# Optimization experiments

Measured on AMD Instinct MI355X. Metric: run time of the kernel, lower is better.

## Reference

```python
import jax, jax.numpy as jnp
import numpy as np


def setup_inputs() -> dict:
    key = jax.random.key(0)
    x = jax.random.normal(key, (2_000_000, 9), dtype=jnp.float32)
    return {"x": x}


def reference(x):
    # Symmetric orthogonalization onto SO(3):
    #   M = U S V^T ;  R = U diag(1, 1, det(U V^T)) V^T
    m = x.reshape(-1, 3, 3)                      # [N, 3, 3]
    u, s, vh = jnp.linalg.svd(m, full_matrices=False)  # u:[N,3,3], vh:[N,3,3] (= V^T)
    det = jnp.linalg.det(jnp.matmul(u, vh))      # [N]
    # Flip last column of U by sign of det to land in SO(3) (det = +1)
    u_fixed = jnp.concatenate(
        [u[:, :, :2], u[:, :, 2:] * det[:, None, None]], axis=2
    )
    return jnp.matmul(u_fixed, vh)               # [N, 3, 3]
```

## Files before the change

kernel.cpp:

```cpp
#include <hip/hip_runtime.h>

#define TPB 256
#define MPW 128
#define FPW (MPW * 9)
#define F4PW (FPW / 4)
#define MPB (MPW * 4)

typedef float v2f __attribute__((ext_vector_type(2)));
typedef int   v2i __attribute__((ext_vector_type(2)));

static __device__ __forceinline__ v2f sqrt2(v2f a){
    v2f r; r.x = __builtin_amdgcn_sqrtf(a.x); r.y = __builtin_amdgcn_sqrtf(a.y); return r;
}
static __device__ __forceinline__ v2f rsq2(v2f a){
    v2f r; r.x = __builtin_amdgcn_rsqf(a.x); r.y = __builtin_amdgcn_rsqf(a.y); return r;
}
static __device__ __forceinline__ v2f csign2(v2f x, v2f y){
    v2f r; r.x = copysignf(x.x, y.x); r.y = copysignf(x.y, y.y); return r;
}
static __device__ __forceinline__ v2f fabs2(v2f x){
    v2f r; r.x = fabsf(x.x); r.y = fabsf(x.y); return r;
}
static __device__ __forceinline__ v2f sel2(v2i m, v2f a, v2f b){
    v2f r; r.x = m.x ? a.x : b.x; r.y = m.y ? a.y : b.y; return r;
}
static __device__ __forceinline__ void rot2(v2f &p, v2f &q, v2f c, v2f s){
    v2f x = p, y = q; p = c*x - s*y; q = s*x + c*y;
}

static __device__ __forceinline__ void jrot2(v2f &app, v2f &aqq, v2f &apq,
                                             v2f &arp, v2f &arq,
                                             v2f &v0p, v2f &v1p, v2f &v2p,
                                             v2f &v0q, v2f &v1q, v2f &v2q)
{
    v2f d   = aqq - app;
    v2f w   = apq + apq;
    v2f nrm = d*d + w*w;
    v2f rr  = sqrt2(nrm);
    v2f sr  = csign2(rr, d);
    v2f den = d + sr;
    v2f inv = rsq2(den*den + w*w);
    v2f c   = fabs2(den) * inv;
    v2f s   = w * csign2(inv, den);
    v2i tiny = nrm < (v2f)1e-30f;
    c = sel2(tiny, (v2f)1.0f, c);
    s = sel2(tiny, (v2f)0.0f, s);
    v2f sum = app + aqq;
    v2f lo  = 0.5f*(sum - sr);
    app = lo; aqq = sum - lo; apq = (v2f)0.0f;
    rot2(arp, arq, c, s);
    rot2(v0p, v0q, c, s);
    rot2(v1p, v1q, c, s);
    rot2(v2p, v2q, c, s);
}

static __device__ __forceinline__ void solve2(
    v2f m00, v2f m01, v2f m02,
    v2f m10, v2f m11, v2f m12,
    v2f m20, v2f m21, v2f m22,
    v2f &r00, v2f &r01, v2f &r02,
    v2f &r10, v2f &r11, v2f &r12,
    v2f &r20, v2f &r21, v2f &r22)
{
    v2f a00 = m00*m00 + m10*m10 + m20*m20;
    v2f a11 = m01*m01 + m11*m11 + m21*m21;
    v2f a22 = m02*m02 + m12*m12 + m22*m22;
    v2f a01 = m00*m01 + m10*m11 + m20*m21;
    v2f a02 = m00*m02 + m10*m12 + m20*m22;
    v2f a12 = m01*m02 + m11*m12 + m21*m22;

    v2f v00 = (v2f)1.0f, v01 = (v2f)0.0f, v02 = (v2f)0.0f;
    v2f v10 = (v2f)0.0f, v11 = (v2f)1.0f, v12 = (v2f)0.0f;
    v2f v20 = (v2f)0.0f, v21 = (v2f)0.0f, v22 = (v2f)1.0f;

    #pragma unroll
    for (int sw = 0; sw < 3; ++sw) {
        jrot2(a00, a11, a01, a02, a12, v00, v10, v20, v01, v11, v21);
        jrot2(a00, a22, a02, a01, a12, v00, v10, v20, v02, v12, v22);
        jrot2(a11, a22, a12, a01, a02, v01, v11, v21, v02, v12, v22);
    }

    v2f t;
    {
        v2i c01 = a00 < a11;
        t = a00; a00 = sel2(c01, a11, a00); a11 = sel2(c01, t, a11);
        t = v00; v00 = sel2(c01, v01, v00); v01 = sel2(c01, -t, v01);
        t = v10; v10 = sel2(c01, v11, v10); v11 = sel2(c01, -t, v11);
        t = v20; v20 = sel2(c01, v21, v20); v21 = sel2(c01, -t, v21);
    }
    {
        v2i c02 = a00 < a22;
        t = a00; a00 = sel2(c02, a22, a00); a22 = sel2(c02, t, a22);
        t = v00; v00 = sel2(c02, v02, v00); v02 = sel2(c02, -t, v02);
        t = v10; v10 = sel2(c02, v12, v10); v12 = sel2(c02, -t, v12);
        t = v20; v20 = sel2(c02, v22, v20); v22 = sel2(c02, -t, v22);
    }
    {
        v2i c12 = a11 < a22;
        t = a11; a11 = sel2(c12, a22, a11); a22 = sel2(c12, t, a22);
        t = v01; v01 = sel2(c12, v02, v01); v02 = sel2(c12, -t, v02);
        t = v11; v11 = sel2(c12, v12, v11); v12 = sel2(c12, -t, v12);
        t = v21; v21 = sel2(c12, v22, v21); v22 = sel2(c12, -t, v22);
    }

    v2f b00 = m00*v00 + m01*v10 + m02*v20;
    v2f b10 = m10*v00 + m11*v10 + m12*v20;
    v2f b20 = m20*v00 + m21*v10 + m22*v20;
    v2f b01 = m00*v01 + m01*v11 + m02*v21;
    v2f b11 = m10*v01 + m11*v11 + m12*v21;
    v2f b21 = m20*v01 + m21*v11 + m22*v21;

    v2f n1 = b00*b00 + b10*b10 + b20*b20;
    v2f i1 = rsq2(n1);
    v2i ok1 = n1 > (v2f)1e-30f;
    i1 = sel2(ok1, i1, (v2f)0.0f);
    v2f u00 = b00*i1, u10 = b10*i1, u20 = b20*i1;

    v2f d12 = b01*u00 + b11*u10 + b21*u20;
    v2f q0 = b01 - d12*u00;
    v2f q1 = b11 - d12*u10;
    v2f q2 = b21 - d12*u20;
    v2f n2 = q0*q0 + q1*q1 + q2*q2;
    v2f i2 = rsq2(n2);
    v2i ok2 = n2 > (v2f)1e-30f;
    i2 = sel2(ok2, i2, (v2f)0.0f);
    v2f u01 = q0*i2, u11 = q1*i2, u21 = q2*i2;

    v2f u02 = u10*u21 - u20*u11;
    v2f u12 = u20*u01 - u00*u21;
    v2f u22 = u00*u11 - u10*u01;

    r00 = u00*v00 + u01*v01 + u02*v02;
    r01 = u00*v10 + u01*v11 + u02*v12;
    r02 = u00*v20 + u01*v21 + u02*v22;
    r10 = u10*v00 + u11*v01 + u12*v02;
    r11 = u10*v10 + u11*v11 + u12*v12;
    r12 = u10*v20 + u11*v21 + u12*v22;
    r20 = u20*v00 + u21*v01 + u22*v02;
    r21 = u20*v10 + u21*v11 + u22*v12;
    r22 = u20*v20 + u21*v21 + u22*v22;
}

static __device__ __forceinline__ float4 ld_f4(const float* __restrict__ x, long f, long ntotf){
    if (f + 4 <= ntotf) return *(const float4*)(x + f);
    float4 r = make_float4(0.f, 0.f, 0.f, 0.f);
    if (f     < ntotf) r.x = x[f];
    if (f + 1 < ntotf) r.y = x[f + 1];
    if (f + 2 < ntotf) r.z = x[f + 2];
    if (f + 3 < ntotf) r.w = x[f + 3];
    return r;
}
static __device__ __forceinline__ void st_f4(float* __restrict__ o, long f, float4 v, long ntotf){
    if (f + 4 <= ntotf) { *(float4*)(o + f) = v; return; }
    if (f     < ntotf) o[f]     = v.x;
    if (f + 1 < ntotf) o[f + 1] = v.y;
    if (f + 2 < ntotf) o[f + 2] = v.z;
    if (f + 3 < ntotf) o[f + 3] = v.w;
}

__global__ __launch_bounds__(TPB) void svdo_kernel(const float* __restrict__ x,
                                                   float* __restrict__ out,
                                                   int nmat)
{
    __shared__ float lds[4][FPW];
    const int lane = threadIdx.x & 63;
    const int wv   = threadIdx.x >> 6;
    const long mbase = (long)blockIdx.x * MPB + (long)wv * MPW;
    const long fb    = mbase * 9;
    const long ntotf = (long)nmat * 9;
    float* L = lds[wv];

    #pragma unroll
    for (int k = 0; k < 5; ++k) {
        const int idx = lane + k * 64;
        if (idx < F4PW) {
            float4 v = ld_f4(x, fb + (long)idx * 4, ntotf);
            *(float4*)&L[idx * 4] = v;
        }
    }
    asm volatile("s_waitcnt lgkmcnt(0)" ::: "memory");
    __builtin_amdgcn_sched_barrier(0);

    const float* p0 = &L[lane * 9];
    const float* p1 = &L[(lane + 64) * 9];
    v2f m00 = {p0[0], p1[0]}, m01 = {p0[1], p1[1]}, m02 = {p0[2], p1[2]};
    v2f m10 = {p0[3], p1[3]}, m11 = {p0[4], p1[4]}, m12 = {p0[5], p1[5]};
    v2f m20 = {p0[6], p1[6]}, m21 = {p0[7], p1[7]}, m22 = {p0[8], p1[8]};

    v2f r00, r01, r02, r10, r11, r12, r20, r21, r22;
    solve2(m00, m01, m02, m10, m11, m12, m20, m21, m22,
           r00, r01, r02, r10, r11, r12, r20, r21, r22);

    float* o0 = &L[lane * 9];
    o0[0]=r00.x; o0[1]=r01.x; o0[2]=r02.x;
    o0[3]=r10.x; o0[4]=r11.x; o0[5]=r12.x;
    o0[6]=r20.x; o0[7]=r21.x; o0[8]=r22.x;
    float* o1 = &L[(lane + 64) * 9];
    o1[0]=r00.y; o1[1]=r01.y; o1[2]=r02.y;
    o1[3]=r10.y; o1[4]=r11.y; o1[5]=r12.y;
    o1[6]=r20.y; o1[7]=r21.y; o1[8]=r22.y;

    asm volatile("s_waitcnt lgkmcnt(0)" ::: "memory");
    __builtin_amdgcn_sched_barrier(0);

    #pragma unroll
    for (int k = 0; k < 5; ++k) {
        const int idx = lane + k * 64;
        if (idx < F4PW) {
            float4 v = *(const float4*)&L[idx * 4];
            st_f4(out, fb + (long)idx * 4, v, ntotf);
        }
    }
}

extern "C" void kernel_launch(void* const* d_in, const int* in_sizes, int n_in,
                              void* d_out, int out_size, void* d_ws, size_t ws_size,
                              hipStream_t stream)
{
    (void)n_in; (void)d_ws; (void)ws_size; (void)out_size;
    const float* x = (const float*)d_in[0];
    float* out = (float*)d_out;
    const int nmat = in_sizes[0] / 9;
    const int grid = (nmat + MPB - 1) / MPB;
    svdo_kernel<<<grid, TPB, 0, stream>>>(x, out, nmat);
}
```

Baseline: 35.72 us.

## Use persistent grid-stride waves with register prefetch of next tile

Replaces the one-tile-per-wave launch with a persistent grid capped at 1024 blocks, where each wave strides over tiles. The next tile's global loads are issued into registers before the current tile's Jacobi SVD runs, so load latency overlaps compute. LDS is doubled to ping-pong two buffers per wave. This adds register pressure and can lower occupancy, and the fixed grid cap may underfill the device or leave tail imbalance.

```diff
diff --git a/kernel.cpp b/kernel.cpp
--- a/kernel.cpp
+++ b/kernel.cpp
@@ -4,7 +4,6 @@
 #define MPW 128
 #define FPW (MPW * 9)
 #define F4PW (FPW / 4)
-#define MPB (MPW * 4)
 
 typedef float v2f __attribute__((ext_vector_type(2)));
 typedef int   v2i __attribute__((ext_vector_type(2)));
@@ -160,56 +159,84 @@
 
 __global__ __launch_bounds__(TPB) void svdo_kernel(const float* __restrict__ x,
                                                    float* __restrict__ out,
-                                                   int nmat)
-{
-    __shared__ float lds[4][FPW];
+                                                   int nmat, int ntiles, int W)
+{
+    __shared__ float lds[4][2 * FPW];
     const int lane = threadIdx.x & 63;
     const int wv   = threadIdx.x >> 6;
-    const long mbase = (long)blockIdx.x * MPB + (long)wv * MPW;
-    const long fb    = mbase * 9;
     const long ntotf = (long)nmat * 9;
-    float* L = lds[wv];
-
-    #pragma unroll
-    for (int k = 0; k < 5; ++k) {
-        const int idx = lane + k * 64;
-        if (idx < F4PW) {
-            float4 v = ld_f4(x, fb + (long)idx * 4, ntotf);
-            *(float4*)&L[idx * 4] = v;
+
+    int tile = blockIdx.x * 4 + wv;
+    if (tile >= ntiles) return;
+
+    float* bufA = &lds[wv][0];
+    float* bufB = &lds[wv][FPW];
+
+    float4 q0, q1, q2, q3, q4;
+    {
+        const long fb = (long)tile * FPW;
+        q0 = ld_f4(x, fb + (long)(lane       ) * 4, ntotf);
+        q1 = ld_f4(x, fb + (long)(lane +  64) * 4, ntotf);
+        q2 = ld_f4(x, fb + (long)(lane + 128) * 4, ntotf);
+        q3 = ld_f4(x, fb + (long)(lane + 192) * 4, ntotf);
+        q4 = make_float4(0.f, 0.f, 0.f, 0.f);
+        if (lane < 32) q4 = ld_f4(x, fb + (long)(lane + 256) * 4, ntotf);
+    }
+
+    for (;;) {
+        *(float4*)&bufA[(lane       ) * 4] = q0;
+        *(float4*)&bufA[(lane +  64) * 4] = q1;
+        *(float4*)&bufA[(lane + 128) * 4] = q2;
+        *(float4*)&bufA[(lane + 192) * 4] = q3;
+        if (lane < 32) *(float4*)&bufA[(lane + 256) * 4] = q4;
+        asm volatile("s_waitcnt lgkmcnt(0)" ::: "memory");
+
+        const int  nxt  = tile + W;
+        const bool have = nxt < ntiles;
+        if (have) {
+            const long fb = (long)nxt * FPW;
+            q0 = ld_f4(x, fb + (long)(lane       ) * 4, ntotf);
+            q1 = ld_f4(x, fb + (long)(lane +  64) * 4, ntotf);
+            q2 = ld_f4(x, fb + (long)(lane + 128) * 4, ntotf);
+            q3 = ld_f4(x, fb + (long)(lane + 192) * 4, ntotf);
+            if (lane < 32) q4 = ld_f4(x, fb + (long)(lane + 256) * 4, ntotf);
         }
-    }
-    asm volatile("s_waitcnt lgkmcnt(0)" ::: "memory");
-    __builtin_amdgcn_sched_barrier(0);
-
-    const float* p0 = &L[lane * 9];
-    const float* p1 = &L[(lane + 64) * 9];
-    v2f m00 = {p0[0], p1[0]}, m01 = {p0[1], p1[1]}, m02 = {p0[2], p1[2]};
-    v2f m10 = {p0[3], p1[3]}, m11 = {p0[4], p1[4]}, m12 = {p0[5], p1[5]};
-    v2f m20 = {p0[6], p1[6]}, m21 = {p0[7], p1[7]}, m22 = {p0[8], p1[8]};
-
-    v2f r00, r01, r02, r10, r11, r12, r20, r21, r22;
-    solve2(m00, m01, m02, m10, m11, m12, m20, m21, m22,
-           r00, r01, r02, r10, r11, r12, r20, r21, r22);
-
-    float* o0 = &L[lane * 9];
-    o0[0]=r00.x; o0[1]=r01.x; o0[2]=r02.x;
-    o0[3]=r10.x; o0[4]=r11.x; o0[5]=r12.x;
-    o0[6]=r20.x; o0[7]=r21.x; o0[8]=r22.x;
-    float* o1 = &L[(lane + 64) * 9];
-    o1[0]=r00.y; o1[1]=r01.y; o1[2]=r02.y;
-    o1[3]=r10.y; o1[4]=r11.y; o1[5]=r12.y;
-    o1[6]=r20.y; o1[7]=r21.y; o1[8]=r22.y;
-
-    asm volatile("s_waitcnt lgkmcnt(0)" ::: "memory");
-    __builtin_amdgcn_sched_barrier(0);
-
-    #pragma unroll
-    for (int k = 0; k < 5; ++k) {
-        const int idx = lane + k * 64;
-        if (idx < F4PW) {
-            float4 v = *(const float4*)&L[idx * 4];
-            st_f4(out, fb + (long)idx * 4, v, ntotf);
+
+        {
+            const float* p0 = &bufA[lane * 9];
+            const float* p1 = &bufA[(lane + 64) * 9];
+            v2f m00 = {p0[0], p1[0]}, m01 = {p0[1], p1[1]}, m02 = {p0[2], p1[2]};
+            v2f m10 = {p0[3], p1[3]}, m11 = {p0[4], p1[4]}, m12 = {p0[5], p1[5]};
+            v2f m20 = {p0[6], p1[6]}, m21 = {p0[7], p1[7]}, m22 = {p0[8], p1[8]};
+
+            v2f r00, r01, r02, r10, r11, r12, r20, r21, r22;
+            solve2(m00, m01, m02, m10, m11, m12, m20, m21, m22,
+                   r00, r01, r02, r10, r11, r12, r20, r21, r22);
+
+            float* o0 = &bufA[lane * 9];
+            o0[0]=r00.x; o0[1]=r01.x; o0[2]=r02.x;
+            o0[3]=r10.x; o0[4]=r11.x; o0[5]=r12.x;
+            o0[6]=r20.x; o0[7]=r21.x; o0[8]=r22.x;
+            float* o1 = &bufA[(lane + 64) * 9];
+            o1[0]=r00.y; o1[1]=r01.y; o1[2]=r02.y;
+            o1[3]=r10.y; o1[4]=r11.y; o1[5]=r12.y;
+            o1[6]=r20.y; o1[7]=r21.y; o1[8]=r22.y;
         }
+        asm volatile("s_waitcnt lgkmcnt(0)" ::: "memory");
+
+        {
+            const long fb = (long)tile * FPW;
+            st_f4(out, fb + (long)(lane       ) * 4, *(const float4*)&bufA[(lane       ) * 4], ntotf);
+            st_f4(out, fb + (long)(lane +  64) * 4, *(const float4*)&bufA[(lane +  64) * 4], ntotf);
+            st_f4(out, fb + (long)(lane + 128) * 4, *(const float4*)&bufA[(lane + 128) * 4], ntotf);
+            st_f4(out, fb + (long)(lane + 192) * 4, *(const float4*)&bufA[(lane + 192) * 4], ntotf);
+            if (lane < 32)
+                st_f4(out, fb + (long)(lane + 256) * 4, *(const float4*)&bufA[(lane + 256) * 4], ntotf);
+        }
+
+        if (!have) break;
+        tile = nxt;
+        float* ts = bufA; bufA = bufB; bufB = ts;
     }
 }
 
@@ -221,6 +248,9 @@
     const float* x = (const float*)d_in[0];
     float* out = (float*)d_out;
     const int nmat = in_sizes[0] / 9;
-    const int grid = (nmat + MPB - 1) / MPB;
-    svdo_kernel<<<grid, TPB, 0, stream>>>(x, out, nmat);
-}
+    const int ntiles = (nmat + MPW - 1) / MPW;
+    int grid = (ntiles + 3) / 4;
+    if (grid > 1024) grid = 1024;
+    const int W = grid * 4;
+    svdo_kernel<<<grid, TPB, 0, stream>>>(x, out, nmat, ntiles, W);
+}
```

New measurement: 33.48 us. 1.07x faster.
